# Performance work log

Hardware: AMD Instinct MI355X
Metric: run time of the kernel (lower is better)

## Reference

```python
import jax, jax.numpy as jnp
import numpy as np

B, S, H, DH, HQ, HKV = 2, 1024, 2048, 128, 16, 4
E, K, I, IS = 16, 4, 1024, 1024
EPS = 1e-5
ROPE_BASE = 10000.0
ROUTED_SCALE = 1.0


def rmsnorm(x, w):
    v = jnp.mean(x.astype(jnp.float32) ** 2, axis=-1, keepdims=True)
    return (x.astype(jnp.float32) * jax.lax.rsqrt(v + EPS)).astype(x.dtype) * w


def rope(x, cos, sin):
    x1, x2 = jnp.split(x, 2, axis=-1)
    return jnp.concatenate([x1 * cos - x2 * sin, x2 * cos + x1 * sin], axis=-1)


def setup_inputs() -> dict:
    key = jax.random.key(0)
    ks = jax.random.split(key, 24)
    s = 0.02
    inp = {}
    inp['x'] = jax.random.normal(ks[0], (B, S, H), dtype=jnp.float32)
    inp['in_ln_w'] = jnp.ones((H,), jnp.float32)
    inp['wq'] = jax.random.normal(ks[1], (H, HQ * DH), jnp.float32) * s
    inp['bq'] = jax.random.normal(ks[2], (HQ * DH,), jnp.float32) * s
    inp['wk'] = jax.random.normal(ks[3], (H, HKV * DH), jnp.float32) * s
    inp['bk'] = jax.random.normal(ks[4], (HKV * DH,), jnp.float32) * s
    inp['wv'] = jax.random.normal(ks[5], (H, HKV * DH), jnp.float32) * s
    inp['bv'] = jax.random.normal(ks[6], (HKV * DH,), jnp.float32) * s
    inp['qn_w'] = jnp.ones((DH,), jnp.float32)
    inp['kn_w'] = jnp.ones((DH,), jnp.float32)
    inp['wo'] = jax.random.normal(ks[7], (HQ * DH, H), jnp.float32) * s
    inp['post_ln_w'] = jnp.ones((H,), jnp.float32)
    inp['gate_w'] = jax.random.normal(ks[8], (E, H), jnp.float32) * s
    inp['gate_b'] = jax.random.normal(ks[9], (E,), jnp.float32) * s
    inp['wg'] = jax.random.normal(ks[10], (E, H, I), jnp.float32) * s
    inp['wu'] = jax.random.normal(ks[11], (E, H, I), jnp.float32) * s
    inp['wd'] = jax.random.normal(ks[12], (E, I, H), jnp.float32) * s
    inp['swg'] = jax.random.normal(ks[13], (H, IS), jnp.float32) * s
    inp['swu'] = jax.random.normal(ks[14], (H, IS), jnp.float32) * s
    inp['swd'] = jax.random.normal(ks[15], (IS, H), jnp.float32) * s
    return inp


def reference(x, in_ln_w, wq, bq, wk, bk, wv, bv, qn_w, kn_w, wo, post_ln_w,
              gate_w, gate_b, wg, wu, wd, swg, swu, swd):
    # ---- attention block ----
    res = x
    h = rmsnorm(x, in_ln_w)
    q = (h @ wq + bq).reshape(B, S, HQ, DH)
    k = (h @ wk + bk).reshape(B, S, HKV, DH)
    v = (h @ wv + bv).reshape(B, S, HKV, DH)
    q = rmsnorm(q, qn_w)  # per-head QK norm over head_dim
    k = rmsnorm(k, kn_w)
    inv_freq = 1.0 / (ROPE_BASE ** (jnp.arange(0, DH, 2, dtype=jnp.float32) / DH))  # [DH/2]
    fr = jnp.arange(S, dtype=jnp.float32)[:, None] * inv_freq[None, :]  # [S, DH/2]
    cos = jnp.cos(fr)[None, :, None, :]
    sin = jnp.sin(fr)[None, :, None, :]
    q = rope(q, cos, sin)
    k = rope(k, cos, sin)
    g = HQ // HKV
    k = jnp.repeat(k, g, axis=2)  # GQA expand to [B,S,HQ,DH]
    v = jnp.repeat(v, g, axis=2)
    scores = jnp.einsum('bqhd,bkhd->bhqk', q, k) * (DH ** -0.5)
    causal = jnp.tril(jnp.ones((S, S), dtype=bool))
    scores = jnp.where(causal[None, None], scores, jnp.float32(-1e30))
    attn = jax.nn.softmax(scores, axis=-1)
    o = jnp.einsum('bhqk,bkhd->bqhd', attn, v).reshape(B, S, HQ * DH) @ wo
    x = res + o
    # ---- MoE block ----
    res = x
    h = rmsnorm(x, post_ln_w)
    ht = h.reshape(B * S, H)  # [T, H]
    logits = ht.astype(jnp.float32) @ gate_w.T  # fp32 router
    scr = jax.nn.sigmoid(logits)  # [T, E]
    choice = scr + gate_b[None, :]  # noaux_tc: bias only for selection
    _, topi = jax.lax.top_k(choice, K)  # [T, K]
    tw = jnp.take_along_axis(scr, topi, axis=-1)  # unbiased combine weights
    tw = tw / (jnp.sum(tw, axis=-1, keepdims=True) + 1e-20)  # norm_topk_prob
    tw = tw * ROUTED_SCALE
    cw = jnp.sum(jax.nn.one_hot(topi, E, dtype=jnp.float32) * tw[..., None], axis=1)  # [T, E]
    a = jnp.einsum('th,ehi->eti', ht, wg)
    b = jnp.einsum('th,ehi->eti', ht, wu)
    inter = jax.nn.silu(a) * b * cw.T[:, :, None]  # scale before down-proj
    routed = jnp.einsum('eti,eih->th', inter, wd)
    shared = (jax.nn.silu(ht @ swg) * (ht @ swu)) @ swd
    out = res + (routed + shared).reshape(B, S, H)
    return out
```

## Files before the change

### kernel.cpp

```cpp
#include <hip/hip_runtime.h>
#include <math.h>

typedef unsigned short u16;
typedef __attribute__((ext_vector_type(8))) short short8;
typedef __attribute__((ext_vector_type(4))) float f32x4;

#define B_ 2
#define S_ 1024
#define H_ 2048
#define DH_ 128
#define HQ_ 16
#define HKV_ 4
#define E_ 16
#define TOPK_ 4
#define I_ 1024
#define T_ (B_*S_)
#define NQKV_ 3072
#define NSEG_ 17
#define NA_ (T_*TOPK_ + T_)
#define K3_ 6144
#define MAXTILE 97

#define QPLANE ((long)B_*HQ_*S_*DH_)
#define KPLANE ((long)B_*HKV_*S_*DH_)
#define VPLANE ((long)B_*HKV_*DH_*S_)

__device__ __forceinline__ float bf2f(u16 u){
  union { unsigned int i; float f; } x; x.i = ((unsigned int)u) << 16; return x.f;
}
__device__ __forceinline__ u16 f2bf(float f){
  union { float f; unsigned int i; } x; x.f = f;
  unsigned int r = x.i + 0x7fffu + ((x.i >> 16) & 1u);
  return (u16)(r >> 16);
}
__device__ __forceinline__ void split_bf(float v, u16& hi, u16& lo){
  hi = f2bf(v);
  lo = f2bf(v - bf2f(hi));
}

__device__ __forceinline__ void gld_lds16(const void* g, void* l){
  __builtin_amdgcn_global_load_lds(
      (const __attribute__((address_space(1))) unsigned int*)g,
      (__attribute__((address_space(3))) unsigned int*)l, 16, 0, 0);
}

__device__ __forceinline__ f32x4 mfma_bf16(short8 a, short8 b, f32x4 c){
  return __builtin_amdgcn_mfma_f32_16x16x32_bf16(a, b, c, 0, 0, 0);
}

__global__ void k_transpose(const float* __restrict__ in, u16* __restrict__ out,
                            int R, int C, int rowMul, int rowOff,
                            long inBatch, long outBatch, int split3)
{
  __shared__ float tile[32][33];
  const float* inp = in + (long)blockIdx.z * inBatch;
  u16* outp = out + (long)blockIdx.z * outBatch;
  int c0 = blockIdx.x * 32, r0 = blockIdx.y * 32;
  int tx = threadIdx.x, ty = threadIdx.y;
#pragma unroll
  for (int i = 0; i < 4; i++)
    tile[ty*4+i][tx] = inp[(long)(r0 + ty*4 + i) * C + c0 + tx];
  __syncthreads();
#pragma unroll
  for (int i = 0; i < 4; i++){
    int c = c0 + ty*4 + i;
    float v = tile[tx][ty*4+i];
    if (split3){
      u16 hi, lo; split_bf(v, hi, lo);
      long base = (long)(c*rowMul + rowOff) * (3*R);
      outp[base + r0 + tx]       = hi;
      outp[base + R + r0 + tx]   = lo;
      outp[base + 2*R + r0 + tx] = hi;
    } else {
      outp[(long)(c*rowMul + rowOff) * R + r0 + tx] = f2bf(v);
    }
  }
}

__global__ void k_rmsnorm(const float* __restrict__ x, const float* __restrict__ w,
                          u16* __restrict__ out3)
{
  int t = blockIdx.x;
  const float4* r4 = (const float4*)(x + (long)t * H_);
  const float4* w4 = (const float4*)w;
  float4 a = r4[threadIdx.x], b = r4[threadIdx.x + 256];
  float ss = a.x*a.x + a.y*a.y + a.z*a.z + a.w*a.w
           + b.x*b.x + b.y*b.y + b.z*b.z + b.w*b.w;
#pragma unroll
  for (int d = 1; d < 64; d <<= 1) ss += __shfl_xor(ss, d);
  __shared__ float red[4];
  int lane = threadIdx.x & 63, wv = threadIdx.x >> 6;
  if (lane == 0) red[wv] = ss;
  __syncthreads();
  ss = red[0] + red[1] + red[2] + red[3];
  float rs = rsqrtf(ss * (1.f / 2048.f) + 1e-5f);
  float4 wa = w4[threadIdx.x], wb = w4[threadIdx.x + 256];
  float va[8] = { a.x*rs*wa.x, a.y*rs*wa.y, a.z*rs*wa.z, a.w*rs*wa.w,
                  b.x*rs*wb.x, b.y*rs*wb.y, b.z*rs*wb.z, b.w*rs*wb.w };
  int pos0 = threadIdx.x*4, pos1 = 1024 + threadIdx.x*4;
  ushort4 hi0, lo0, hi1, lo1;
  split_bf(va[0], hi0.x, lo0.x); split_bf(va[1], hi0.y, lo0.y);
  split_bf(va[2], hi0.z, lo0.z); split_bf(va[3], hi0.w, lo0.w);
  split_bf(va[4], hi1.x, lo1.x); split_bf(va[5], hi1.y, lo1.y);
  split_bf(va[6], hi1.z, lo1.z); split_bf(va[7], hi1.w, lo1.w);
  u16* row = out3 + (long)t * K3_;
  *(ushort4*)(row + pos0) = hi0;        *(ushort4*)(row + pos1) = hi1;
  *(ushort4*)(row + 2048 + pos0) = hi0; *(ushort4*)(row + 2048 + pos1) = hi1;
  *(ushort4*)(row + 4096 + pos0) = lo0; *(ushort4*)(row + 4096 + pos1) = lo1;
}

__global__ void k_add_rmsnorm(const float* __restrict__ x, const float* __restrict__ p0,
                              const float* __restrict__ p1, const float* __restrict__ p2,
                              const float* __restrict__ w, float* __restrict__ xa,
                              u16* __restrict__ out1, float* __restrict__ outf)
{
  int t = blockIdx.x;
  long base = (long)t * H_;
  const float4* x4 = (const float4*)(x + base);
  const float4* a4 = (const float4*)(p0 + base);
  const float4* b4 = (const float4*)(p1 + base);
  const float4* c4 = (const float4*)(p2 + base);
  const float4* w4 = (const float4*)w;
  int i0 = threadIdx.x, i1 = threadIdx.x + 256;
  float4 xv0 = x4[i0], xv1 = x4[i1];
  float4 av0 = a4[i0], av1 = a4[i1];
  float4 bv0 = b4[i0], bv1 = b4[i1];
  float4 cv0 = c4[i0], cv1 = c4[i1];
  float4 s0, s1;
  s0.x = xv0.x+av0.x+bv0.x+cv0.x; s0.y = xv0.y+av0.y+bv0.y+cv0.y;
  s0.z = xv0.z+av0.z+bv0.z+cv0.z; s0.w = xv0.w+av0.w+bv0.w+cv0.w;
  s1.x = xv1.x+av1.x+bv1.x+cv1.x; s1.y = xv1.y+av1.y+bv1.y+cv1.y;
  s1.z = xv1.z+av1.z+bv1.z+cv1.z; s1.w = xv1.w+av1.w+bv1.w+cv1.w;
  *(float4*)(xa + base + i0*4) = s0;
  *(float4*)(xa + base + i1*4) = s1;
  float ss = s0.x*s0.x + s0.y*s0.y + s0.z*s0.z + s0.w*s0.w
           + s1.x*s1.x + s1.y*s1.y + s1.z*s1.z + s1.w*s1.w;
#pragma unroll
  for (int d = 1; d < 64; d <<= 1) ss += __shfl_xor(ss, d);
  __shared__ float red[4];
  int lane = threadIdx.x & 63, wv = threadIdx.x >> 6;
  if (lane == 0) red[wv] = ss;
  __syncthreads();
  ss = red[0] + red[1] + red[2] + red[3];
  float rs = rsqrtf(ss * (1.f / 2048.f) + 1e-5f);
  float4 wa = w4[i0], wb = w4[i1];
  float va[8] = { s0.x*rs*wa.x, s0.y*rs*wa.y, s0.z*rs*wa.z, s0.w*rs*wa.w,
                  s1.x*rs*wb.x, s1.y*rs*wb.y, s1.z*rs*wb.z, s1.w*rs*wb.w };
  ushort4 q0 = { f2bf(va[0]), f2bf(va[1]), f2bf(va[2]), f2bf(va[3]) };
  ushort4 q1 = { f2bf(va[4]), f2bf(va[5]), f2bf(va[6]), f2bf(va[7]) };
  *(ushort4*)(out1 + base + i0*4) = q0;
  *(ushort4*)(out1 + base + i1*4) = q1;
  float4 oa = { va[0], va[1], va[2], va[3] };
  float4 ob = { va[4], va[5], va[6], va[7] };
  *(float4*)(outf + base + i0*4) = oa;
  *(float4*)(outf + base + i1*4) = ob;
}

__global__ void k_ropetab(float* __restrict__ tab){
  int s = blockIdx.x, i = threadIdx.x;
  double inv = pow(10000.0, -(double)i / 64.0);
  double fr = (double)s * inv;
  tab[s*128 + i]      = (float)cos(fr);
  tab[s*128 + 64 + i] = (float)sin(fr);
}

__global__ void k_ropenorm(const float* __restrict__ qkv0, const float* __restrict__ qkv1,
                           const float* __restrict__ biascat,
                           const float* __restrict__ qnw, const float* __restrict__ knw,
                           const float* __restrict__ tab,
                           u16* __restrict__ Q, u16* __restrict__ Kn, u16* __restrict__ Vt)
{
  long gw = (long)blockIdx.x * 4 + (threadIdx.x >> 6);
  int lane = threadIdx.x & 63;
  int hr = (int)(gw % 24);
  long bs = gw / 24;
  int s = (int)(bs % S_);
  int b = (int)(bs / S_);
  long ro = bs * NQKV_ + hr * DH_;
  float x1 = qkv0[ro + lane] + qkv1[ro + lane] + biascat[hr*DH_ + lane];
  float x2 = qkv0[ro + lane + 64] + qkv1[ro + lane + 64] + biascat[hr*DH_ + lane + 64];
  if (hr < 20){
    float ss = x1*x1 + x2*x2;
#pragma unroll
    for (int d = 1; d < 64; d <<= 1) ss += __shfl_xor(ss, d);
    float rs = rsqrtf(ss * (1.f/128.f) + 1e-5f);
    const float* wn = (hr < 16) ? qnw : knw;
    float y1 = x1 * rs * wn[lane], y2 = x2 * rs * wn[lane + 64];
    float c = tab[s*128 + lane], sn = tab[s*128 + 64 + lane];
    float o1 = y1*c - y2*sn, o2 = y2*c + y1*sn;
    if (hr < 16){
      const float sc = 0.088388347648318447f;
      u16 h1,l1,h2,l2;
      split_bf(o1*sc, h1, l1); split_bf(o2*sc, h2, l2);
      u16* dst = Q + (((long)b*HQ_ + hr)*S_ + s) * DH_;
      dst[lane] = h1; dst[lane+64] = h2;
      dst[QPLANE + lane] = l1; dst[QPLANE + lane+64] = l2;
    } else {
      u16 h1,l1,h2,l2;
      split_bf(o1, h1, l1); split_bf(o2, h2, l2);
      u16* dst = Kn + (((long)b*HKV_ + (hr-16))*S_ + s) * DH_;
      dst[lane] = h1; dst[lane+64] = h2;
      dst[KPLANE + lane] = l1; dst[KPLANE + lane+64] = l2;
    }
  } else {
    u16 h1,l1,h2,l2;
    split_bf(x1, h1, l1); split_bf(x2, h2, l2);
    u16* dst = Vt + (((long)b*HKV_ + (hr-20))*DH_) * S_ + s;
    dst[(long)lane * S_]        = h1;
    dst[(long)(lane + 64) * S_] = h2;
    dst[VPLANE + (long)lane * S_]        = l1;
    dst[VPLANE + (long)(lane + 64) * S_] = l2;
  }
}

__launch_bounds__(256)
__global__ void k_attn(const u16* __restrict__ Q, const u16* __restrict__ Kn,
                       const u16* __restrict__ Vt, u16* __restrict__ O3)
{
  __shared__ u16 Ksh[32][128];
  __shared__ u16 Ksl[32][128];
  __shared__ u16 Vsh[128][32];
  __shared__ u16 Vsl[128][32];
  __shared__ u16 Psh[4][16][40];
  __shared__ u16 Psl[4][16][40];
  int qb = blockIdx.x, h = blockIdx.y, b = blockIdx.z;
  int kvh = h >> 2;
  int q0 = qb * 64;
  int tid = threadIdx.x, lane = tid & 63, w = tid >> 6;

  const u16* Qg = Q  + (((long)b*HQ_  + h  )*S_ + q0) * DH_;
  const u16* Kg = Kn + (((long)b*HKV_ + kvh)*S_) * DH_;
  const u16* Vg = Vt + (((long)b*HKV_ + kvh)*DH_) * S_;

  short8 qh[4], ql[4];
  {
    long qrow = w*16 + (lane & 15);
    int coff = (lane >> 4) << 3;
#pragma unroll
    for (int kst = 0; kst < 4; kst++){
      qh[kst] = *(const short8*)(Qg + qrow*DH_ + kst*32 + coff);
      ql[kst] = *(const short8*)(Qg + QPLANE + qrow*DH_ + kst*32 + coff);
    }
  }

  f32x4 o[8];
#pragma unroll
  for (int nt = 0; nt < 8; nt++) o[nt] = (f32x4){0.f,0.f,0.f,0.f};
  float mrow[4] = {-INFINITY,-INFINITY,-INFINITY,-INFINITY};
  float lrow[4] = {0.f,0.f,0.f,0.f};

  for (int j = 0; j <= 2*qb + 1; ++j){
#pragma unroll
    for (int it = 0; it < 2; ++it){
      int flat = it*256 + tid;
      int r = flat >> 4, pc = flat & 15;
      int c = pc ^ (((r&7) << 1) | ((r >> 3) & 1));
      long gsrc = ((long)(j*32 + r))*DH_ + c*8;
      gld_lds16(Kg + gsrc,          &Ksh[0][0] + (it*256 + (w<<6))*8);
      gld_lds16(Kg + KPLANE + gsrc, &Ksl[0][0] + (it*256 + (w<<6))*8);
    }
#pragma unroll
    for (int it = 0; it < 2; ++it){
      int flat = it*256 + tid;
      int r = flat >> 2, pc = flat & 3;
      int c = pc ^ (r & 3);
      long gsrc = (long)r*S_ + j*32 + c*8;
      gld_lds16(Vg + gsrc,          &Vsh[0][0] + (it*256 + (w<<6))*8);
      gld_lds16(Vg + VPLANE + gsrc, &Vsl[0][0] + (it*256 + (w<<6))*8);
    }
    __syncthreads();

    f32x4 s[2];
#pragma unroll
    for (int nt = 0; nt < 2; nt++) s[nt] = (f32x4){0.f,0.f,0.f,0.f};
#pragma unroll
    for (int kst = 0; kst < 4; kst++){
#pragma unroll
      for (int nt = 0; nt < 2; nt++){
        int br = nt*16 + (lane & 15);
        int bc = (kst*4 + (lane >> 4)) ^ (((br&7)<<1) | ((br>>3)&1));
        short8 kh = *(const short8*)&Ksh[br][bc*8];
        short8 kl = *(const short8*)&Ksl[br][bc*8];
        s[nt] = mfma_bf16(qh[kst], kh, s[nt]);
        s[nt] = mfma_bf16(qh[kst], kl, s[nt]);
        s[nt] = mfma_bf16(ql[kst], kh, s[nt]);
      }
    }
    if (j >= 2*qb){
#pragma unroll
      for (int nt = 0; nt < 2; nt++){
        int key = j*32 + nt*16 + (lane & 15);
#pragma unroll
        for (int r = 0; r < 4; r++){
          int qrow = q0 + w*16 + ((lane >> 4) << 2) + r;
          if (key > qrow) s[nt][r] = -1e30f;
        }
      }
    }
    float pm[4];
#pragma unroll
    for (int r = 0; r < 4; r++) pm[r] = fmaxf(s[0][r], s[1][r]);
#pragma unroll
    for (int d = 1; d < 16; d <<= 1){
#pragma unroll
      for (int r = 0; r < 4; r++) pm[r] = fmaxf(pm[r], __shfl_xor(pm[r], d));
    }
    float alpha[4];
#pragma unroll
    for (int r = 0; r < 4; r++){
      float mn = fmaxf(mrow[r], pm[r]);
      alpha[r] = __expf(mrow[r] - mn);
      mrow[r] = mn;
    }
    float psum[4] = {0.f,0.f,0.f,0.f};
#pragma unroll
    for (int nt = 0; nt < 2; nt++){
#pragma unroll
      for (int r = 0; r < 4; r++){
        float p = __expf(s[nt][r] - mrow[r]);
        psum[r] += p;
        u16 ph, pl; split_bf(p, ph, pl);
        int qr = ((lane>>4)<<2) + r, kc = nt*16 + (lane & 15);
        Psh[w][qr][kc] = ph;
        Psl[w][qr][kc] = pl;
      }
    }
#pragma unroll
    for (int d = 1; d < 16; d <<= 1){
#pragma unroll
      for (int r = 0; r < 4; r++) psum[r] += __shfl_xor(psum[r], d);
    }
#pragma unroll
    for (int r = 0; r < 4; r++) lrow[r] = lrow[r]*alpha[r] + psum[r];
#pragma unroll
    for (int nt = 0; nt < 8; nt++)
#pragma unroll
      for (int r = 0; r < 4; r++) o[nt][r] *= alpha[r];

    {
      short8 pah = *(const short8*)&Psh[w][lane & 15][(lane >> 4) << 3];
      short8 pal = *(const short8*)&Psl[w][lane & 15][(lane >> 4) << 3];
#pragma unroll
      for (int nt = 0; nt < 8; nt++){
        int br = nt*16 + (lane & 15);
        int bc = (lane >> 4) ^ (br & 3);
        short8 vh = *(const short8*)&Vsh[br][bc*8];
        short8 vl = *(const short8*)&Vsl[br][bc*8];
        o[nt] = mfma_bf16(pah, vh, o[nt]);
        o[nt] = mfma_bf16(pah, vl, o[nt]);
        o[nt] = mfma_bf16(pal, vh, o[nt]);
      }
    }
    __syncthreads();
  }
  float inv_[4];
#pragma unroll
  for (int r = 0; r < 4; r++) inv_[r] = 1.f / lrow[r];
#pragma unroll
  for (int nt = 0; nt < 8; nt++){
#pragma unroll
    for (int r = 0; r < 4; r++){
      long row = (long)b*S_ + q0 + w*16 + ((lane >> 4) << 2) + r;
      float val = o[nt][r] * inv_[r];
      u16 hi, lo; split_bf(val, hi, lo);
      long base = row*K3_ + h*DH_ + nt*16 + (lane & 15);
      O3[base]        = hi;
      O3[base + 2048] = hi;
      O3[base + 4096] = lo;
    }
  }
}

template<int MODE>
__launch_bounds__(256)
__global__ void k_gemm(const u16* __restrict__ A, const u16* __restrict__ Bm,
                       void* __restrict__ Cout,
                       int M, int N, int Kloop, int Kstride, long segStrideB,
                       const int* __restrict__ segStart, const int* __restrict__ segCount,
                       const int* __restrict__ tileSeg, const int* __restrict__ tileMb,
                       const int* __restrict__ meta,
                       const int* __restrict__ assignTS, const float* __restrict__ assignW,
                       u16* __restrict__ downb)
{
  __shared__ u16 As[128][64];
  __shared__ u16 Bs[128][64];
  int tid = threadIdx.x;
  int lane = tid & 63, w = tid >> 6;
  int wr = w >> 1, wc = w & 1;
  int n0 = blockIdx.x * 128;
  int seg = 0, m0, segBase = 0, cnt = M, kbase = 0;
  long outOff = 0;
  if constexpr (MODE >= 2){
    int ty = blockIdx.y;
    if (ty >= meta[0]) return;
    seg = tileSeg[ty]; m0 = tileMb[ty] * 128;
    segBase = segStart[seg];
    cnt = segCount[seg];
  } else {
    m0 = blockIdx.y * 128;
    kbase = blockIdx.z * Kloop;
    outOff = (long)blockIdx.z * M * N;
  }
  const u16* Bp = Bm + (long)seg * segStrideB;

  const u16* aS[4]; const u16* bS[4];
#pragma unroll
  for (int it = 0; it < 4; ++it){
    int flat = it*256 + tid;
    int r = flat >> 3, pc = flat & 7;
    int c = pc ^ (r & 7);
    long arow;
    if constexpr (MODE == 2) arow = (long)(assignTS[segBase + m0 + r] >> 3);
    else if constexpr (MODE == 3) arow = (long)(segBase + m0 + r);
    else arow = (long)(m0 + r);
    aS[it] = A + arow * Kstride + kbase + c*8;
    bS[it] = Bp + (long)(n0 + r) * Kstride + kbase + c*8;
  }

  f32x4 acc[4][4];
#pragma unroll
  for (int m = 0; m < 4; m++)
#pragma unroll
    for (int n = 0; n < 4; n++) acc[m][n] = (f32x4){0.f,0.f,0.f,0.f};

  u16* AsF = &As[0][0]; u16* BsF = &Bs[0][0];
  for (int k0 = 0; k0 < Kloop; k0 += 64){
#pragma unroll
    for (int it = 0; it < 4; ++it){
      gld_lds16(aS[it] + k0, AsF + (it*256 + (w<<6))*8);
      gld_lds16(bS[it] + k0, BsF + (it*256 + (w<<6))*8);
    }
    __syncthreads();
#pragma unroll
    for (int kh = 0; kh < 2; ++kh){
      short8 af[4], bfv[4];
#pragma unroll
      for (int m = 0; m < 4; m++){
        int r = wr*64 + m*16 + (lane & 15);
        int c = (kh*4 + (lane >> 4)) ^ (r & 7);
        af[m] = *(const short8*)&As[r][c*8];
      }
#pragma unroll
      for (int n = 0; n < 4; n++){
        int r = wc*64 + n*16 + (lane & 15);
        int c = (kh*4 + (lane >> 4)) ^ (r & 7);
        bfv[n] = *(const short8*)&Bs[r][c*8];
      }
#pragma unroll
      for (int m = 0; m < 4; m++)
#pragma unroll
        for (int n = 0; n < 4; n++)
          acc[m][n] = mfma_bf16(af[m], bfv[n], acc[m][n]);
    }
    __syncthreads();
  }

  if constexpr (MODE == 0 || MODE == 1){
    float* C = (float*)Cout + outOff;
#pragma unroll
    for (int m = 0; m < 4; m++){
      int row0 = m0 + wr*64 + m*16 + ((lane >> 4) << 2);
#pragma unroll
      for (int n = 0; n < 4; n++){
        int col = n0 + wc*64 + n*16 + (lane & 15);
#pragma unroll
        for (int r = 0; r < 4; r++)
          C[(long)(row0 + r)*N + col] = acc[m][n][r];
      }
    }
  } else if constexpr (MODE == 2){
    u16* inter = (u16*)Cout;
#pragma unroll
    for (int m = 0; m < 4; m++){
      int row0 = m0 + wr*64 + m*16 + ((lane >> 4) << 2);
#pragma unroll
      for (int n = 0; n < 4; n++){
        f32x4 a = acc[m][n];
        float ov[4];
#pragma unroll
        for (int r = 0; r < 4; r++) ov[r] = __shfl_xor(a[r], 1);
        if ((lane & 1) == 0){
          int colp = (n0 + wc*64 + n*16 + (lane & 15)) >> 1;
#pragma unroll
          for (int r = 0; r < 4; r++){
            int rl = row0 + r;
            if (rl < cnt){
              int pos = segBase + rl;
              float g = a[r], u = ov[r];
              float val = (g / (1.f + __expf(-g))) * u * assignW[pos];
              inter[(long)pos*I_ + colp] = f2bf(val);
            }
          }
        }
      }
    }
  } else {
#pragma unroll
    for (int m = 0; m < 4; m++){
      int row0 = m0 + wr*64 + m*16 + ((lane >> 4) << 2);
#pragma unroll
      for (int n = 0; n < 4; n++){
        int col = n0 + wc*64 + n*16 + (lane & 15);
#pragma unroll
        for (int r = 0; r < 4; r++){
          int rl = row0 + r;
          if (rl < cnt){
            int ts = assignTS[segBase + rl];
            downb[((long)(ts >> 3)*5 + (ts & 7))*H_ + col] = f2bf(acc[m][n][r]);
          }
        }
      }
    }
  }
}

__global__ void k_router(const float* __restrict__ ht, const float* __restrict__ gw,
                         const float* __restrict__ gb, int* __restrict__ tok_e,
                         float* __restrict__ tok_w, int* __restrict__ counts)
{
  int t = blockIdx.x * 4 + (threadIdx.x >> 6);
  int lane = threadIdx.x & 63;
  const float4* row4 = (const float4*)(ht + (long)t * H_);
  float acc[16];
#pragma unroll
  for (int e = 0; e < 16; e++) acc[e] = 0.f;
#pragma unroll
  for (int it = 0; it < 8; it++){
    float4 rv = row4[lane + 64*it];
#pragma unroll
    for (int e = 0; e < 16; e++){
      float4 gv = *(const float4*)(gw + (long)e*H_ + (lane + 64*it)*4);
      acc[e] += rv.x*gv.x + rv.y*gv.y + rv.z*gv.z + rv.w*gv.w;
    }
  }
#pragma unroll
  for (int d = 1; d < 64; d <<= 1){
#pragma unroll
    for (int e = 0; e < 16; e++) acc[e] += __shfl_xor(acc[e], d);
  }
  if (lane == 0){
    float scr[16], ch[16];
#pragma unroll
    for (int e = 0; e < 16; e++){
      float s = 1.f / (1.f + __expf(-acc[e]));
      scr[e] = s; ch[e] = s + gb[e];
    }
    int sel[4]; float tw[4]; float sum = 0.f;
#pragma unroll
    for (int k = 0; k < 4; k++){
      int best = -1; float bv = -1e30f;
      for (int e = 0; e < 16; e++){
        bool used = false;
        for (int j = 0; j < k; j++) if (sel[j] == e) used = true;
        if (!used && ch[e] > bv){ bv = ch[e]; best = e; }
      }
      sel[k] = best; tw[k] = scr[best]; sum += scr[best];
    }
    float inv = 1.f / (sum + 1e-20f);
#pragma unroll
    for (int k = 0; k < 4; k++){
      tok_e[t*4 + k] = sel[k];
      tok_w[t*4 + k] = tw[k] * inv;
      atomicAdd(&counts[sel[k]], 1);
    }
  }
}

__global__ void k_scan(const int* __restrict__ counts, int* __restrict__ segStart,
                       int* __restrict__ segCount, int* __restrict__ cursor,
                       int* __restrict__ tileSeg, int* __restrict__ tileMb,
                       int* __restrict__ meta)
{
  if (threadIdx.x == 0){
    int off = 0, nt = 0;
    for (int e = 0; e < 16; e++){
      segStart[e] = off; segCount[e] = counts[e]; cursor[e] = off;
      for (int mb = 0; mb*128 < counts[e]; ++mb){ tileSeg[nt] = e; tileMb[nt] = mb; nt++; }
      off += counts[e];
    }
    segStart[16] = T_*TOPK_; segCount[16] = T_;
    for (int mb = 0; mb < 16; ++mb){ tileSeg[nt] = 16; tileMb[nt] = mb; nt++; }
    meta[0] = nt;
  }
}

__global__ void k_scatter(const int* __restrict__ tok_e, const float* __restrict__ tok_w,
                          int* __restrict__ cursor, int* __restrict__ assignTS,
                          float* __restrict__ assignW)
{
  int t = blockIdx.x*256 + threadIdx.x;
  if (t < T_){
    for (int k = 0; k < 4; k++){
      int e = tok_e[t*4 + k];
      int pos = atomicAdd(&cursor[e], 1);
      assignTS[pos] = t*8 + k;
      assignW[pos] = tok_w[t*4 + k];
    }
    assignTS[T_*TOPK_ + t] = t*8 + 4;
    assignW[T_*TOPK_ + t] = 1.f;
  }
}

__global__ void k_final(const float* __restrict__ xa, const u16* __restrict__ downb,
                        float* __restrict__ out)
{
  long i = ((long)blockIdx.x*256 + threadIdx.x) * 4;
  int t = (int)(i >> 11);
  int h = (int)(i & 2047);
  float4 r = *(const float4*)(xa + i);
  float a0 = r.x, a1 = r.y, a2 = r.z, a3 = r.w;
#pragma unroll
  for (int k = 0; k < 5; k++){
    const u16* d = downb + ((long)t*5 + k)*H_ + h;
    ushort4 v = *(const ushort4*)d;
    a0 += bf2f(v.x); a1 += bf2f(v.y); a2 += bf2f(v.z); a3 += bf2f(v.w);
  }
  float4 o = { a0, a1, a2, a3 };
  *(float4*)(out + i) = o;
}

extern "C" void kernel_launch(void* const* d_in, const int* in_sizes, int n_in,
                              void* d_out, int out_size, void* d_ws, size_t ws_size,
                              hipStream_t stream)
{
  (void)in_sizes; (void)n_in; (void)out_size; (void)ws_size;
  const float* x      = (const float*)d_in[0];
  const float* inlnw  = (const float*)d_in[1];
  const float* wq     = (const float*)d_in[2];
  const float* bq     = (const float*)d_in[3];
  const float* wk     = (const float*)d_in[4];
  const float* bk     = (const float*)d_in[5];
  const float* wv     = (const float*)d_in[6];
  const float* bv     = (const float*)d_in[7];
  const float* qnw    = (const float*)d_in[8];
  const float* knw    = (const float*)d_in[9];
  const float* wo     = (const float*)d_in[10];
  const float* postln = (const float*)d_in[11];
  const float* gatew  = (const float*)d_in[12];
  const float* gateb  = (const float*)d_in[13];
  const float* wg     = (const float*)d_in[14];
  const float* wu     = (const float*)d_in[15];
  const float* wdp    = (const float*)d_in[16];
  const float* swg    = (const float*)d_in[17];
  const float* swu    = (const float*)d_in[18];
  const float* swd    = (const float*)d_in[19];
  float* out = (float*)d_out;

  char* ws = (char*)d_ws;
  size_t off = 0;
  auto alloc = [&](size_t bytes) -> char* {
    char* p = ws + off; off += (bytes + 255) & ~(size_t)255; return p;
  };
  u16*   wqkv2   = (u16*)  alloc((size_t)NQKV_*K3_*2);
  u16*   wo2     = (u16*)  alloc((size_t)H_*K3_*2);
  u16*   wgu_t   = (u16*)  alloc((size_t)NSEG_*2048*2048*2);
  u16*   wd_t    = (u16*)  alloc((size_t)NSEG_*2048*1024*2);
  float* tab     = (float*)alloc((size_t)S_*128*4);
  float* biascat = (float*)alloc((size_t)NQKV_*4);
  float* xa      = (float*)alloc((size_t)T_*H_*4);
  int*   tok_e   = (int*)  alloc((size_t)T_*4*4);
  float* tok_w   = (float*)alloc((size_t)T_*4*4);
  int*   counts  = (int*)  alloc(32*4);
  int*   segStart= (int*)  alloc(32*4);
  int*   segCount= (int*)  alloc(32*4);
  int*   cursor  = (int*)  alloc(32*4);
  int*   tileSeg = (int*)  alloc(128*4);
  int*   tileMb  = (int*)  alloc(128*4);
  int*   meta    = (int*)  alloc(32*4);
  int*   assignTS= (int*)  alloc((size_t)NA_*4);
  float* assignW = (float*)alloc((size_t)NA_*4);
  char*  scrA    = alloc((size_t)T_*K3_*2);
  char*  scrBC   = alloc((size_t)2*T_*NQKV_*4);
  char*  scrD    = alloc((size_t)(2*QPLANE + 2*KPLANE + 2*VPLANE)*2);

  u16*   h2      = (u16*)scrA;
  u16*   attno2  = (u16*)scrA;
  u16*   inter   = (u16*)scrA;
  float* qkvp0   = (float*)scrBC;
  float* qkvp1   = (float*)(scrBC + (size_t)T_*NQKV_*4);
  float* wop     = (float*)scrBC;
  u16*   Qb2     = (u16*)scrD;
  u16*   Kn2     = (u16*)(scrD + (size_t)2*QPLANE*2);
  u16*   Vt2     = (u16*)(scrD + (size_t)2*QPLANE*2 + (size_t)2*KPLANE*2);
  float* ht_f    = (float*)scrD;
  u16*   ht_b    = (u16*)(scrD + (size_t)T_*H_*4);
  u16*   downb   = (u16*)scrD;

  dim3 tb(32, 8);
  k_transpose<<<dim3(64,64,1),  tb, 0, stream>>>(wq,  wqkv2, 2048, 2048, 1, 0,    0, 0, 1);
  k_transpose<<<dim3(16,64,1),  tb, 0, stream>>>(wk,  wqkv2, 2048, 512,  1, 2048, 0, 0, 1);
  k_transpose<<<dim3(16,64,1),  tb, 0, stream>>>(wv,  wqkv2, 2048, 512,  1, 2560, 0, 0, 1);
  k_transpose<<<dim3(64,64,1),  tb, 0, stream>>>(wo,  wo2,   2048, 2048, 1, 0,    0, 0, 1);
  k_transpose<<<dim3(32,64,16), tb, 0, stream>>>(wg,  wgu_t, 2048, 1024, 2, 0, (long)2048*1024, (long)2048*2048, 0);
  k_transpose<<<dim3(32,64,16), tb, 0, stream>>>(wu,  wgu_t, 2048, 1024, 2, 1, (long)2048*1024, (long)2048*2048, 0);
  k_transpose<<<dim3(32,64,1),  tb, 0, stream>>>(swg, wgu_t + (long)16*2048*2048, 2048, 1024, 2, 0, 0, 0, 0);
  k_transpose<<<dim3(32,64,1),  tb, 0, stream>>>(swu, wgu_t + (long)16*2048*2048, 2048, 1024, 2, 1, 0, 0, 0);
  k_transpose<<<dim3(64,32,16), tb, 0, stream>>>(wdp, wd_t,  1024, 2048, 1, 0, (long)1024*2048, (long)2048*1024, 0);
  k_transpose<<<dim3(64,32,1),  tb, 0, stream>>>(swd, wd_t + (long)16*2048*1024, 1024, 2048, 1, 0, 0, 0, 0);

  hipMemcpyAsync(biascat,        bq, 2048*4, hipMemcpyDeviceToDevice, stream);
  hipMemcpyAsync(biascat + 2048, bk, 512*4,  hipMemcpyDeviceToDevice, stream);
  hipMemcpyAsync(biascat + 2560, bv, 512*4,  hipMemcpyDeviceToDevice, stream);

  k_ropetab<<<S_, 64, 0, stream>>>(tab);
  k_rmsnorm<<<T_, 256, 0, stream>>>(x, inlnw, h2);

  k_gemm<0><<<dim3(24,16,2), 256, 0, stream>>>(h2, wqkv2, qkvp0, T_, NQKV_,
      K3_/2, K3_, 0, nullptr, nullptr, nullptr, nullptr, nullptr, nullptr, nullptr, nullptr);

  k_ropenorm<<<(T_*24)/4, 256, 0, stream>>>(qkvp0, qkvp1, biascat, qnw, knw, tab, Qb2, Kn2, Vt2);

  k_attn<<<dim3(S_/64, HQ_, B_), 256, 0, stream>>>(Qb2, Kn2, Vt2, attno2);

  k_gemm<1><<<dim3(16,16,3), 256, 0, stream>>>(attno2, wo2, wop, T_, H_,
      K3_/3, K3_, 0, nullptr, nullptr, nullptr, nullptr, nullptr, nullptr, nullptr, nullptr);

  k_add_rmsnorm<<<T_, 256, 0, stream>>>(x, wop, wop + (long)T_*H_, wop + (long)2*T_*H_,
      postln, xa, ht_b, ht_f);

  hipMemsetAsync(counts, 0, 32*4, stream);
  k_router<<<T_/4, 256, 0, stream>>>(ht_f, gatew, gateb, tok_e, tok_w, counts);
  k_scan<<<1, 64, 0, stream>>>(counts, segStart, segCount, cursor, tileSeg, tileMb, meta);
  k_scatter<<<(T_+255)/256, 256, 0, stream>>>(tok_e, tok_w, cursor, assignTS, assignW);

  k_gemm<2><<<dim3(16,MAXTILE,1), 256, 0, stream>>>(ht_b, wgu_t, inter, 0, 2048,
      H_, H_, (long)2048*2048, segStart, segCount, tileSeg, tileMb, meta, assignTS, assignW, nullptr);

  k_gemm<3><<<dim3(16,MAXTILE,1), 256, 0, stream>>>(inter, wd_t, nullptr, 0, H_,
      I_, I_, (long)2048*1024, segStart, segCount, tileSeg, tileMb, meta, assignTS, assignW, downb);

  k_final<<<(T_*H_/4)/256, 256, 0, stream>>>(xa, downb, out);
}
```

Measured before the change: 913.1 us.

## Pipeline GEMM K-loop with 4-stage LDS ring and drop split-K partials

Rewrites the bf16 MFMA GEMM main loop to use a four-deep ring of 32-wide K tiles in LDS. Loads are issued three stages ahead and gated with explicit vmcnt waits and barriers, with the K trip count made a compile-time template parameter. The QKV and output-projection GEMMs no longer split K across blockIdx.z, so the consumers read one buffer instead of summing two or three. This aims to hide global-load latency and remove the extra partial-sum traffic. In exchange, the dense GEMMs now launch fewer blocks, each doing a longer serial K loop.

```diff
diff --git a/kernel.cpp b/kernel.cpp
--- a/kernel.cpp
+++ b/kernel.cpp
@@ -110,7 +110,6 @@
 }
 
 __global__ void k_add_rmsnorm(const float* __restrict__ x, const float* __restrict__ p0,
-                              const float* __restrict__ p1, const float* __restrict__ p2,
                               const float* __restrict__ w, float* __restrict__ xa,
                               u16* __restrict__ out1, float* __restrict__ outf)
 {
@@ -118,19 +117,13 @@
   long base = (long)t * H_;
   const float4* x4 = (const float4*)(x + base);
   const float4* a4 = (const float4*)(p0 + base);
-  const float4* b4 = (const float4*)(p1 + base);
-  const float4* c4 = (const float4*)(p2 + base);
   const float4* w4 = (const float4*)w;
   int i0 = threadIdx.x, i1 = threadIdx.x + 256;
   float4 xv0 = x4[i0], xv1 = x4[i1];
   float4 av0 = a4[i0], av1 = a4[i1];
-  float4 bv0 = b4[i0], bv1 = b4[i1];
-  float4 cv0 = c4[i0], cv1 = c4[i1];
   float4 s0, s1;
-  s0.x = xv0.x+av0.x+bv0.x+cv0.x; s0.y = xv0.y+av0.y+bv0.y+cv0.y;
-  s0.z = xv0.z+av0.z+bv0.z+cv0.z; s0.w = xv0.w+av0.w+bv0.w+cv0.w;
-  s1.x = xv1.x+av1.x+bv1.x+cv1.x; s1.y = xv1.y+av1.y+bv1.y+cv1.y;
-  s1.z = xv1.z+av1.z+bv1.z+cv1.z; s1.w = xv1.w+av1.w+bv1.w+cv1.w;
+  s0.x = xv0.x+av0.x; s0.y = xv0.y+av0.y; s0.z = xv0.z+av0.z; s0.w = xv0.w+av0.w;
+  s1.x = xv1.x+av1.x; s1.y = xv1.y+av1.y; s1.z = xv1.z+av1.z; s1.w = xv1.w+av1.w;
   *(float4*)(xa + base + i0*4) = s0;
   *(float4*)(xa + base + i1*4) = s1;
   float ss = s0.x*s0.x + s0.y*s0.y + s0.z*s0.z + s0.w*s0.w
@@ -164,8 +157,7 @@
   tab[s*128 + 64 + i] = (float)sin(fr);
 }
 
-__global__ void k_ropenorm(const float* __restrict__ qkv0, const float* __restrict__ qkv1,
-                           const float* __restrict__ biascat,
+__global__ void k_ropenorm(const float* __restrict__ qkv, const float* __restrict__ biascat,
                            const float* __restrict__ qnw, const float* __restrict__ knw,
                            const float* __restrict__ tab,
                            u16* __restrict__ Q, u16* __restrict__ Kn, u16* __restrict__ Vt)
@@ -177,8 +169,8 @@
   int s = (int)(bs % S_);
   int b = (int)(bs / S_);
   long ro = bs * NQKV_ + hr * DH_;
-  float x1 = qkv0[ro + lane] + qkv1[ro + lane] + biascat[hr*DH_ + lane];
-  float x2 = qkv0[ro + lane + 64] + qkv1[ro + lane + 64] + biascat[hr*DH_ + lane + 64];
+  float x1 = qkv[ro + lane] + biascat[hr*DH_ + lane];
+  float x2 = qkv[ro + lane + 64] + biascat[hr*DH_ + lane + 64];
   if (hr < 20){
     float ss = x1*x1 + x2*x2;
 #pragma unroll
@@ -371,25 +363,23 @@
   }
 }
 
-template<int MODE>
+template<int MODE, int KITERS>
 __launch_bounds__(256)
 __global__ void k_gemm(const u16* __restrict__ A, const u16* __restrict__ Bm,
                        void* __restrict__ Cout,
-                       int M, int N, int Kloop, int Kstride, long segStrideB,
+                       int N, int Kstride, long segStrideB,
                        const int* __restrict__ segStart, const int* __restrict__ segCount,
                        const int* __restrict__ tileSeg, const int* __restrict__ tileMb,
                        const int* __restrict__ meta,
                        const int* __restrict__ assignTS, const float* __restrict__ assignW,
                        u16* __restrict__ downb)
 {
-  __shared__ u16 As[128][64];
-  __shared__ u16 Bs[128][64];
+  __shared__ u16 LDS[4*8192];
   int tid = threadIdx.x;
   int lane = tid & 63, w = tid >> 6;
   int wr = w >> 1, wc = w & 1;
   int n0 = blockIdx.x * 128;
-  int seg = 0, m0, segBase = 0, cnt = M, kbase = 0;
-  long outOff = 0;
+  int seg = 0, m0, segBase = 0, cnt = 1 << 30;
   if constexpr (MODE >= 2){
     int ty = blockIdx.y;
     if (ty >= meta[0]) return;
@@ -398,23 +388,35 @@
     cnt = segCount[seg];
   } else {
     m0 = blockIdx.y * 128;
-    kbase = blockIdx.z * Kloop;
-    outOff = (long)blockIdx.z * M * N;
   }
   const u16* Bp = Bm + (long)seg * segStrideB;
 
-  const u16* aS[4]; const u16* bS[4];
-#pragma unroll
-  for (int it = 0; it < 4; ++it){
-    int flat = it*256 + tid;
-    int r = flat >> 3, pc = flat & 7;
-    int c = pc ^ (r & 7);
+  const u16* aS[2]; const u16* bS[2];
+#pragma unroll
+  for (int it = 0; it < 2; ++it){
+    int c = w + it*4;
+    int row = c*16 + (lane >> 2);
+    int ps = (lane & 3) ^ ((row >> 1) & 3);
     long arow;
-    if constexpr (MODE == 2) arow = (long)(assignTS[segBase + m0 + r] >> 3);
-    else if constexpr (MODE == 3) arow = (long)(segBase + m0 + r);
-    else arow = (long)(m0 + r);
-    aS[it] = A + arow * Kstride + kbase + c*8;
-    bS[it] = Bp + (long)(n0 + r) * Kstride + kbase + c*8;
+    if constexpr (MODE == 2) arow = (long)(assignTS[segBase + m0 + row] >> 3);
+    else if constexpr (MODE == 3) arow = (long)(segBase + m0 + row);
+    else arow = (long)(m0 + row);
+    aS[it] = A + arow * Kstride + ps*8;
+    bS[it] = Bp + (long)(n0 + row) * Kstride + ps*8;
+  }
+
+  int offA[4], offB[4];
+#pragma unroll
+  for (int m = 0; m < 4; m++){
+    int r = wr*64 + m*16 + (lane & 15);
+    int ps = (lane >> 4) ^ ((r >> 1) & 3);
+    offA[m] = r*32 + ps*8;
+  }
+#pragma unroll
+  for (int n = 0; n < 4; n++){
+    int r = wc*64 + n*16 + (lane & 15);
+    int ps = (lane >> 4) ^ ((r >> 1) & 3);
+    offB[n] = 4096 + r*32 + ps*8;
   }
 
   f32x4 acc[4][4];
@@ -423,40 +425,45 @@
 #pragma unroll
     for (int n = 0; n < 4; n++) acc[m][n] = (f32x4){0.f,0.f,0.f,0.f};
 
-  u16* AsF = &As[0][0]; u16* BsF = &Bs[0][0];
-  for (int k0 = 0; k0 < Kloop; k0 += 64){
-#pragma unroll
-    for (int it = 0; it < 4; ++it){
-      gld_lds16(aS[it] + k0, AsF + (it*256 + (w<<6))*8);
-      gld_lds16(bS[it] + k0, BsF + (it*256 + (w<<6))*8);
-    }
-    __syncthreads();
-#pragma unroll
-    for (int kh = 0; kh < 2; ++kh){
-      short8 af[4], bfv[4];
-#pragma unroll
-      for (int m = 0; m < 4; m++){
-        int r = wr*64 + m*16 + (lane & 15);
-        int c = (kh*4 + (lane >> 4)) ^ (r & 7);
-        af[m] = *(const short8*)&As[r][c*8];
-      }
-#pragma unroll
-      for (int n = 0; n < 4; n++){
-        int r = wc*64 + n*16 + (lane & 15);
-        int c = (kh*4 + (lane >> 4)) ^ (r & 7);
-        bfv[n] = *(const short8*)&Bs[r][c*8];
-      }
-#pragma unroll
-      for (int m = 0; m < 4; m++)
-#pragma unroll
-        for (int n = 0; n < 4; n++)
-          acc[m][n] = mfma_bf16(af[m], bfv[n], acc[m][n]);
-    }
-    __syncthreads();
-  }
-
-  if constexpr (MODE == 0 || MODE == 1){
-    float* C = (float*)Cout + outOff;
+  auto STAGE = [&](int Tt){
+    int kb = Tt * 32;
+    int db = (Tt & 3) * 8192;
+#pragma unroll
+    for (int it = 0; it < 2; ++it){
+      gld_lds16(aS[it] + kb, &LDS[db + (w + it*4)*512]);
+      gld_lds16(bS[it] + kb, &LDS[db + 4096 + (w + it*4)*512]);
+    }
+  };
+
+  STAGE(0); STAGE(1); STAGE(2);
+
+  for (int T = 0; T < KITERS; ++T){
+    if (T + 3 < KITERS) STAGE(T + 3);
+    int rem = KITERS - 1 - T;
+    if (rem >= 3)      asm volatile("s_waitcnt vmcnt(12)" ::: "memory");
+    else if (rem == 2) asm volatile("s_waitcnt vmcnt(8)"  ::: "memory");
+    else if (rem == 1) asm volatile("s_waitcnt vmcnt(4)"  ::: "memory");
+    else               asm volatile("s_waitcnt vmcnt(0)"  ::: "memory");
+    __builtin_amdgcn_s_barrier();
+    __builtin_amdgcn_sched_barrier(0);
+    const u16* L = &LDS[(T & 3) * 8192];
+    short8 af[4], bfv[4];
+#pragma unroll
+    for (int m = 0; m < 4; m++) af[m]  = *(const short8*)(L + offA[m]);
+#pragma unroll
+    for (int n = 0; n < 4; n++) bfv[n] = *(const short8*)(L + offB[n]);
+#pragma unroll
+    for (int m = 0; m < 4; m++)
+#pragma unroll
+      for (int n = 0; n < 4; n++)
+        acc[m][n] = mfma_bf16(af[m], bfv[n], acc[m][n]);
+    asm volatile("s_waitcnt lgkmcnt(0)" ::: "memory");
+    __builtin_amdgcn_sched_barrier(0);
+    __builtin_amdgcn_s_barrier();
+  }
+
+  if constexpr (MODE == 0){
+    float* C = (float*)Cout;
 #pragma unroll
     for (int m = 0; m < 4; m++){
       int row0 = m0 + wr*64 + m*16 + ((lane >> 4) << 2);
@@ -677,7 +684,6 @@
   u16*   attno2  = (u16*)scrA;
   u16*   inter   = (u16*)scrA;
   float* qkvp0   = (float*)scrBC;
-  float* qkvp1   = (float*)(scrBC + (size_t)T_*NQKV_*4);
   float* wop     = (float*)scrBC;
   u16*   Qb2     = (u16*)scrD;
   u16*   Kn2     = (u16*)(scrD + (size_t)2*QPLANE*2);
@@ -705,29 +711,28 @@
   k_ropetab<<<S_, 64, 0, stream>>>(tab);
   k_rmsnorm<<<T_, 256, 0, stream>>>(x, inlnw, h2);
 
-  k_gemm<0><<<dim3(24,16,2), 256, 0, stream>>>(h2, wqkv2, qkvp0, T_, NQKV_,
-      K3_/2, K3_, 0, nullptr, nullptr, nullptr, nullptr, nullptr, nullptr, nullptr, nullptr);
-
-  k_ropenorm<<<(T_*24)/4, 256, 0, stream>>>(qkvp0, qkvp1, biascat, qnw, knw, tab, Qb2, Kn2, Vt2);
+  k_gemm<0,192><<<dim3(24,16), 256, 0, stream>>>(h2, wqkv2, qkvp0,
+      NQKV_, K3_, 0, nullptr, nullptr, nullptr, nullptr, nullptr, nullptr, nullptr, nullptr);
+
+  k_ropenorm<<<(T_*24)/4, 256, 0, stream>>>(qkvp0, biascat, qnw, knw, tab, Qb2, Kn2, Vt2);
 
   k_attn<<<dim3(S_/64, HQ_, B_), 256, 0, stream>>>(Qb2, Kn2, Vt2, attno2);
 
-  k_gemm<1><<<dim3(16,16,3), 256, 0, stream>>>(attno2, wo2, wop, T_, H_,
-      K3_/3, K3_, 0, nullptr, nullptr, nullptr, nullptr, nullptr, nullptr, nullptr, nullptr);
-
-  k_add_rmsnorm<<<T_, 256, 0, stream>>>(x, wop, wop + (long)T_*H_, wop + (long)2*T_*H_,
-      postln, xa, ht_b, ht_f);
+  k_gemm<0,192><<<dim3(16,16), 256, 0, stream>>>(attno2, wo2, wop,
+      H_, K3_, 0, nullptr, nullptr, nullptr, nullptr, nullptr, nullptr, nullptr, nullptr);
+
+  k_add_rmsnorm<<<T_, 256, 0, stream>>>(x, wop, postln, xa, ht_b, ht_f);
 
   hipMemsetAsync(counts, 0, 32*4, stream);
   k_router<<<T_/4, 256, 0, stream>>>(ht_f, gatew, gateb, tok_e, tok_w, counts);
   k_scan<<<1, 64, 0, stream>>>(counts, segStart, segCount, cursor, tileSeg, tileMb, meta);
   k_scatter<<<(T_+255)/256, 256, 0, stream>>>(tok_e, tok_w, cursor, assignTS, assignW);
 
-  k_gemm<2><<<dim3(16,MAXTILE,1), 256, 0, stream>>>(ht_b, wgu_t, inter, 0, 2048,
-      H_, H_, (long)2048*2048, segStart, segCount, tileSeg, tileMb, meta, assignTS, assignW, nullptr);
-
-  k_gemm<3><<<dim3(16,MAXTILE,1), 256, 0, stream>>>(inter, wd_t, nullptr, 0, H_,
-      I_, I_, (long)2048*1024, segStart, segCount, tileSeg, tileMb, meta, assignTS, assignW, downb);
+  k_gemm<2,64><<<dim3(16,MAXTILE), 256, 0, stream>>>(ht_b, wgu_t, inter,
+      2048, H_, (long)2048*2048, segStart, segCount, tileSeg, tileMb, meta, assignTS, assignW, nullptr);
+
+  k_gemm<3,32><<<dim3(16,MAXTILE), 256, 0, stream>>>(inter, wd_t, nullptr,
+      H_, I_, (long)2048*1024, segStart, segCount, tileSeg, tileMb, meta, assignTS, assignW, downb);
 
   k_final<<<(T_*H_/4)/256, 256, 0, stream>>>(xa, downb, out);
 }
```

After: 899.8 us. About the same (-1.5%).
